# Kernel tuning notes

Hardware: AMD Instinct MI355X
Metric: run time of the kernel (lower is better)

Reference implementation:

```python
import jax, jax.numpy as jnp
import numpy as np

B, C_IN, H, W = 64, 2048, 14, 14
D, FF, G, NC, NH = 768, 2048, 100, 9605, 8
DF = int(NC / G + 0.999)  # 97
HD = D // NH
EPS = 1e-5


def _ln(x, g, b):
    m = jnp.mean(x, axis=-1, keepdims=True)
    v = jnp.mean(jnp.square(x - m), axis=-1, keepdims=True)
    return (x - m) * jax.lax.rsqrt(v + EPS) * g + b


def setup_inputs() -> dict:
    key = jax.random.key(0)
    ks = jax.random.split(key, 16)
    def xav(k, shape):
        fan_in, fan_out = shape[-1], shape[-2] if len(shape) > 1 else shape[-1]
        std = float(np.sqrt(2.0 / (fan_in + fan_out)))
        return jax.random.normal(k, shape, jnp.float32) * std
    return {
        "x": jax.random.normal(ks[0], (B, C_IN, H, W), jnp.float32),
        "w_embed": xav(ks[1], (D, C_IN)), "b_embed": jnp.zeros((D,), jnp.float32),
        "query_embed": jax.random.normal(ks[2], (G, D), jnp.float32),
        "wq": xav(ks[3], (D, D)), "bq": jnp.zeros((D,), jnp.float32),
        "wk": xav(ks[4], (D, D)), "bk": jnp.zeros((D,), jnp.float32),
        "wv": xav(ks[5], (D, D)), "bv": jnp.zeros((D,), jnp.float32),
        "wo": xav(ks[6], (D, D)), "bo": jnp.zeros((D,), jnp.float32),
        "g1": jnp.ones((D,), jnp.float32), "be1": jnp.zeros((D,), jnp.float32),
        "g2": jnp.ones((D,), jnp.float32), "be2": jnp.zeros((D,), jnp.float32),
        "g3": jnp.ones((D,), jnp.float32), "be3": jnp.zeros((D,), jnp.float32),
        "w1": xav(ks[7], (FF, D)), "bl1": jnp.zeros((FF,), jnp.float32),
        "w2": xav(ks[8], (D, FF)), "bl2": jnp.zeros((D,), jnp.float32),
        "dup_pool": xav(ks[9], (G, D, DF)),
        "dup_bias": jnp.zeros((NC,), jnp.float32),
    }


def reference(x, w_embed, b_embed, query_embed, wq, bq, wk, bk, wv, bv, wo, bo,
              g1, be1, g2, be2, g3, be3, w1, bl1, w2, bl2, dup_pool, dup_bias):
    bs = x.shape[0]
    # [B, C, H, W] -> [B, S, C]
    mem = x.reshape(bs, x.shape[1], -1).transpose(0, 2, 1)
    # embed_standart + relu -> [B, S, D]
    mem = jax.nn.relu(jnp.einsum('bsc,dc->bsd', mem, w_embed) + b_embed)
    # tgt = queries broadcast to batch: [B, G, D]
    tgt = jnp.broadcast_to(query_embed[None], (bs, G, D))
    # layer: tgt = norm1(tgt + dropout1(tgt)) = norm1(2*tgt)
    tgt = _ln(tgt + tgt, g1, be1)
    # cross multihead attention (q=tgt, k=v=mem)
    q = (jnp.einsum('bgd,ed->bge', tgt, wq) + bq).reshape(bs, G, NH, HD)
    k = (jnp.einsum('bsd,ed->bse', mem, wk) + bk).reshape(bs, -1, NH, HD)
    v = (jnp.einsum('bsd,ed->bse', mem, wv) + bv).reshape(bs, -1, NH, HD)
    scores = jnp.einsum('bghd,bshd->bhgs', q, k) / jnp.sqrt(jnp.float32(HD))
    attn = jax.nn.softmax(scores, axis=-1)
    ctx = jnp.einsum('bhgs,bshd->bghd', attn, v).reshape(bs, G, D)
    ctx = jnp.einsum('bgd,ed->bge', ctx, wo) + bo
    tgt = _ln(tgt + ctx, g2, be2)
    # FFN
    ff = jax.nn.relu(jnp.einsum('bgd,fd->bgf', tgt, w1) + bl1)
    ff = jnp.einsum('bgf,df->bgd', ff, w2) + bl2
    h = _ln(tgt + ff, g3, be3)  # [B, G, D]
    # grouped FC: per-group matmul fused into one batched einsum
    out_extrap = jnp.einsum('bgd,gdf->bgf', h, dup_pool)  # [B, G, DF]
    logits = out_extrap.reshape(bs, G * DF)[:, :NC] + dup_bias
    return logits
```

## Files before the change

kernel.cpp:

```cpp
#include <hip/hip_runtime.h>
#include <hip/hip_bf16.h>


#define B_    64
#define CIN_  2048
#define S_    196
#define D_    768
#define FF_   2048
#define G_    100
#define NC_   9605
#define NH_   8
#define HD_   96
#define DF_   97
#define FP_   112
#define GP_   112
#define SP_   224
#define BS_   (B_ * S_)
#define BG_   (B_ * G_)

typedef __bf16 bf16x8 __attribute__((ext_vector_type(8)));
typedef float  f32x4  __attribute__((ext_vector_type(4)));
typedef ushort us8    __attribute__((ext_vector_type(8)));

__device__ __forceinline__ float bf2f(ushort u) {
  union { unsigned int i; float f; } v; v.i = ((unsigned int)u) << 16; return v.f;
}
__device__ __forceinline__ ushort f2bf(float f) {
  __hip_bfloat16 h = __float2bfloat16(f);
  return *reinterpret_cast<ushort*>(&h);
}

__device__ __forceinline__ void gl2lds16(const ushort* g, ushort* l) {
  __builtin_amdgcn_global_load_lds((const __attribute__((address_space(1))) unsigned int*)g,
                                   (__attribute__((address_space(3))) unsigned int*)l, 16, 0, 0);
}

#define DT_BLKS 400
#define XP_BLKS 2048
#define CV_BLKS 512
#define TG_BLKS 128

struct PrepArgs {
  const float* x;   ushort* aemb;
  const float* dup; ushort* dupT;
  const float* csrc[7]; ushort* cdst[7]; int cn4[7]; int ctotal;
  const float* qe; const float* g1; const float* be1;
  float* tgt; ushort* tgtB;
};

__global__ __launch_bounds__(256) void k_prep(PrepArgs pa) {
  __shared__ __align__(16) char smem[196 * 72 * 2];
  int jid = blockIdx.x;
  const int t = threadIdx.x;

  if (jid < DT_BLKS) {
    float (*tile)[33] = (float (*)[33])smem;
    const int g = jid >> 2, dchunk = jid & 3;
    const int tx = t & 31, ty = t >> 5;
    for (int di = 0; di < 6; ++di) {
      const int d0 = dchunk * 192 + di * 32;
      for (int f0 = 0; f0 < 128; f0 += 32) {
        #pragma unroll
        for (int r = 0; r < 32; r += 8) {
          int d = d0 + ty + r, f = f0 + tx;
          tile[ty + r][tx] = (f < DF_) ? pa.dup[(size_t)g * D_ * DF_ + (size_t)d * DF_ + f] : 0.f;
        }
        __syncthreads();
        #pragma unroll
        for (int r = 0; r < 32; r += 8) {
          int f = f0 + ty + r, d = d0 + tx;
          if (f < FP_) pa.dupT[((size_t)g * FP_ + f) * D_ + d] = f2bf(tile[tx][ty + r]);
        }
        __syncthreads();
      }
    }
    return;
  }
  jid -= DT_BLKS;

  if (jid < XP_BLKS) {
    ushort* xs = (ushort*)smem;
    const int b = jid >> 5, cbase = (jid & 31) * 64;
    const float* xb = pa.x + ((size_t)b * CIN_ + cbase) * S_;
    #pragma unroll
    for (int it = 0; it < 4; ++it) {
      const int u = it * 256 + t;
      if (u < 784) {
        const int cq = u / 49, j = u - cq * 49;
        const int s = 4 * j;
        float4 a[4];
        #pragma unroll
        for (int r = 0; r < 4; ++r)
          a[r] = *(const float4*)(xb + (size_t)(cq * 4 + r) * S_ + s);
        #pragma unroll
        for (int r = 0; r < 4; ++r) {
          ushort4 o;
          o.x = f2bf(((const float*)&a[0])[r]);
          o.y = f2bf(((const float*)&a[1])[r]);
          o.z = f2bf(((const float*)&a[2])[r]);
          o.w = f2bf(((const float*)&a[3])[r]);
          *(ushort4*)&xs[(s + r) * 72 + cq * 4] = o;
        }
      }
    }
    __syncthreads();
    const int sl = t >> 3, oct = t & 7;
    #pragma unroll
    for (int sr = 0; sr < 7; ++sr) {
      const int s = sr * 32 + sl;
      if (s < S_) {
        us8 v = *(const us8*)&xs[s * 72 + oct * 8];
        *(us8*)&pa.aemb[((size_t)(b * S_ + s)) * CIN_ + cbase + oct * 8] = v;
      }
    }
    return;
  }
  jid -= XP_BLKS;

  if (jid < CV_BLKS) {
    int i = jid * 256 + t;
    const int stride = CV_BLKS * 256;
    for (; i < pa.ctotal; i += stride) {
      int seg = 0, off = i;
      while (off >= pa.cn4[seg]) { off -= pa.cn4[seg]; ++seg; }
      const float4* sp = (const float4*)pa.csrc[seg];
      float4 v0 = sp[2 * off], v1 = sp[2 * off + 1];
      us8 o;
      o[0] = f2bf(v0.x); o[1] = f2bf(v0.y); o[2] = f2bf(v0.z); o[3] = f2bf(v0.w);
      o[4] = f2bf(v1.x); o[5] = f2bf(v1.y); o[6] = f2bf(v1.z); o[7] = f2bf(v1.w);
      ((us8*)pa.cdst[seg])[off] = o;
    }
    return;
  }
  jid -= CV_BLKS;

  float* r1 = (float*)smem;
  float* r2 = r1 + 256;
  const int g = jid;
  if (g >= G_) {
    for (int d = t; d < D_; d += 256) pa.tgtB[(size_t)g * D_ + d] = 0;
    return;
  }
  float y[3]; float s = 0.f, sq = 0.f;
  const float* row = pa.qe + (size_t)g * D_;
  #pragma unroll
  for (int i = 0; i < 3; ++i) { float v = 2.f * row[t + i * 256]; y[i] = v; s += v; sq += v * v; }
  r1[t] = s; r2[t] = sq; __syncthreads();
  for (int o = 128; o > 0; o >>= 1) { if (t < o) { r1[t] += r1[t + o]; r2[t] += r2[t + o]; } __syncthreads(); }
  const float mean = r1[0] * (1.f / D_);
  const float var  = r2[0] * (1.f / D_) - mean * mean;
  const float w = rsqrtf(var + 1e-5f);
  #pragma unroll
  for (int i = 0; i < 3; ++i) {
    int d = t + i * 256;
    float v = (y[i] - mean) * w * pa.g1[d] + pa.be1[d];
    pa.tgt[(size_t)g * D_ + d] = v;
    pa.tgtB[(size_t)g * D_ + d] = f2bf(v);
  }
}

__device__ __forceinline__ void gemm_core(const ushort* __restrict__ A, const ushort* __restrict__ B,
    const float* __restrict__ bias, const float* __restrict__ bias2,
    float* __restrict__ Cf, ushort* __restrict__ Cb, ushort* __restrict__ Vt,
    int N, int K, int m0, int n0, int relu, ushort* As, ushort* Bs) {
  const int t = threadIdx.x;
  const int lane = t & 63, wave = t >> 6;
  const int quad = lane >> 4, lrow = lane & 15;
  const int wr = (wave >> 1) * 64, wc = (wave & 1) * 64;
  const int srow = t >> 2, scol = (t & 3) * 8;
  f32x4 acc[4][4] = {};
  for (int k0 = 0; k0 < K; k0 += 32) {
    const ushort* ag = A + (size_t)(m0 + srow) * K + k0 + scol;
    const ushort* bg = B + (size_t)(n0 + srow) * K + k0 + scol;
    gl2lds16(ag,                    &As[srow * 32 + scol]);
    gl2lds16(ag + (size_t)64 * K,   &As[(srow + 64) * 32 + scol]);
    gl2lds16(bg,                    &Bs[srow * 32 + scol]);
    gl2lds16(bg + (size_t)64 * K,   &Bs[(srow + 64) * 32 + scol]);
    __syncthreads();
    bf16x8 af[4], bfr[4];
    #pragma unroll
    for (int i = 0; i < 4; ++i) af[i] = *(const bf16x8*)&As[(wr + i * 16 + lrow) * 32 + quad * 8];
    #pragma unroll
    for (int j = 0; j < 4; ++j) bfr[j] = *(const bf16x8*)&Bs[(wc + j * 16 + lrow) * 32 + quad * 8];
    #pragma unroll
    for (int i = 0; i < 4; ++i)
      #pragma unroll
      for (int j = 0; j < 4; ++j)
        acc[i][j] = __builtin_amdgcn_mfma_f32_16x16x32_bf16(af[i], bfr[j], acc[i][j], 0, 0, 0);
    __syncthreads();
  }
  #pragma unroll
  for (int i = 0; i < 4; ++i) {
    #pragma unroll
    for (int j = 0; j < 4; ++j) {
      const int gcol = n0 + wc + j * 16 + lrow;
      const float bv = (bias2 && gcol >= D_) ? bias2[gcol - D_] : (bias ? bias[gcol] : 0.f);
      if (Vt && gcol >= D_) {
        const int dv = gcol - D_, hh = dv / HD_, hd = dv % HD_;
        const int row0 = m0 + wr + i * 16 + quad * 4;
        const int bb = row0 / S_, ss = row0 % S_;
        ushort4 o;
        o.x = f2bf(acc[i][j][0] + bv);
        o.y = f2bf(acc[i][j][1] + bv);
        o.z = f2bf(acc[i][j][2] + bv);
        o.w = f2bf(acc[i][j][3] + bv);
        *(ushort4*)&Vt[((size_t)(bb * NH_ + hh) * HD_ + hd) * SP_ + ss] = o;
      } else {
        #pragma unroll
        for (int r = 0; r < 4; ++r) {
          const int grow = m0 + wr + i * 16 + quad * 4 + r;
          float v = acc[i][j][r] + bv;
          if (relu) v = fmaxf(v, 0.f);
          if (Cf) Cf[(size_t)grow * N + gcol] = v;
          else    Cb[(size_t)grow * N + gcol] = f2bf(v);
        }
      }
    }
  }
}

__global__ __launch_bounds__(256) void k_gemm(const ushort* __restrict__ A, const ushort* __restrict__ B,
    const float* __restrict__ bias, const float* __restrict__ bias2,
    float* __restrict__ Cf, ushort* __restrict__ Cb, ushort* __restrict__ Vt,
    int N, int K, int nbx, int nm, int relu,
    const ushort* __restrict__ A2, const ushort* __restrict__ B2,
    const float* __restrict__ bias_2, ushort* __restrict__ Cb2, int N2, int K2) {
  __shared__ ushort As[128 * 32];
  __shared__ ushort Bs[128 * 32];
  const int l = blockIdx.x;
  const int base = ((nm + 7) & ~7) * nbx;
  if (l >= base) {
    gemm_core(A2, B2, bias_2, nullptr, nullptr, Cb2, nullptr, N2, K2, 0, (l - base) * 128, 0, As, Bs);
    return;
  }
  const int mb = (l >> 3) / nbx * 8 + (l & 7);
  const int nb = (l >> 3) % nbx;
  if (mb >= nm) return;
  gemm_core(A, B, bias, bias2, Cf, Cb, Vt, N, K, mb * 128, nb * 128, relu, As, Bs);
}
static inline int swz_grid(int nm, int nbx) { return ((nm + 7) & ~7) * nbx; }

__device__ __forceinline__ void gemm_core64(const ushort* __restrict__ A, const ushort* __restrict__ B,
    const float* __restrict__ bias, ushort* __restrict__ Cb,
    int N, int K, int m0, int n0, int relu, ushort* As, ushort* Bs) {
  const int t = threadIdx.x;
  const int lane = t & 63, wave = t >> 6;
  const int quad = lane >> 4, lrow = lane & 15;
  const int wr = (wave >> 1) * 32, wc = (wave & 1) * 64;
  const int srow = t >> 2, scol = (t & 3) * 8;
  f32x4 acc[2][4] = {};
  for (int k0 = 0; k0 < K; k0 += 32) {
    const ushort* ag = A + (size_t)(m0 + srow) * K + k0 + scol;
    const ushort* bg = B + (size_t)(n0 + srow) * K + k0 + scol;
    gl2lds16(ag,                  &As[srow * 32 + scol]);
    gl2lds16(bg,                  &Bs[srow * 32 + scol]);
    gl2lds16(bg + (size_t)64 * K, &Bs[(srow + 64) * 32 + scol]);
    __syncthreads();
    bf16x8 af[2], bfr[4];
    #pragma unroll
    for (int i = 0; i < 2; ++i) af[i] = *(const bf16x8*)&As[(wr + i * 16 + lrow) * 32 + quad * 8];
    #pragma unroll
    for (int j = 0; j < 4; ++j) bfr[j] = *(const bf16x8*)&Bs[(wc + j * 16 + lrow) * 32 + quad * 8];
    #pragma unroll
    for (int i = 0; i < 2; ++i)
      #pragma unroll
      for (int j = 0; j < 4; ++j)
        acc[i][j] = __builtin_amdgcn_mfma_f32_16x16x32_bf16(af[i], bfr[j], acc[i][j], 0, 0, 0);
    __syncthreads();
  }
  #pragma unroll
  for (int i = 0; i < 2; ++i) {
    #pragma unroll
    for (int j = 0; j < 4; ++j) {
      const int gcol = n0 + wc + j * 16 + lrow;
      const float bv = bias ? bias[gcol] : 0.f;
      #pragma unroll
      for (int r = 0; r < 4; ++r) {
        const int grow = m0 + wr + i * 16 + quad * 4 + r;
        float v = acc[i][j][r] + bv;
        if (relu) v = fmaxf(v, 0.f);
        Cb[(size_t)grow * N + gcol] = f2bf(v);
      }
    }
  }
}

__global__ __launch_bounds__(256) void k_gemm64(const ushort* __restrict__ A, const ushort* __restrict__ B,
    const float* __restrict__ bias, ushort* __restrict__ Cb,
    int N, int K, int nbx, int nm, int relu,
    const ushort* __restrict__ A2, const ushort* __restrict__ B2,
    const float* __restrict__ bias_2, ushort* __restrict__ Cb2, int N2, int K2, int nbx2) {
  __shared__ ushort As[64 * 32];
  __shared__ ushort Bs[128 * 32];
  const int l = blockIdx.x;
  const int base = ((nm + 7) & ~7) * nbx;
  if (l >= base) {
    const int l2 = l - base;
    gemm_core64(A2, B2, bias_2, Cb2, N2, K2, (l2 / nbx2) * 64, (l2 % nbx2) * 128, 0, As, Bs);
    return;
  }
  const int mb = (l >> 3) / nbx * 8 + (l & 7);
  const int nb = (l >> 3) % nbx;
  if (mb >= nm) return;
  gemm_core64(A, B, bias, Cb, N, K, mb * 64, nb * 128, relu, As, Bs);
}

__global__ __launch_bounds__(256) void k_attn(const ushort* __restrict__ qB,
    const ushort* __restrict__ Kb, const ushort* __restrict__ VbT, ushort* __restrict__ ctx) {
  __shared__ ushort lds[GP_ * SP_];
  ushort* Ks = lds;
  ushort* Ps = lds;
  const int h = blockIdx.x, b = blockIdx.y, t = threadIdx.x;
  const int bh = b * NH_ + h;
  const int lane = t & 63, wave = t >> 6;
  const int quad = lane >> 4, c = lane & 15;
  for (int i = t; i < 208 * 12; i += 256) {
    int r = i / 12, col = (i % 12) * 8;
    gl2lds16(Kb + ((size_t)(b * S_ + r)) * D_ + h * HD_ + col, &Ks[i * 8]);
  }
  __syncthreads();
  const float scale = 0.1020620726f;
  f32x4 p[2][13];
  #pragma unroll
  for (int rep = 0; rep < 2; ++rep) {
    const int ii = wave + rep * 4;
    if (ii >= 7) continue;
    bf16x8 af[3];
    #pragma unroll
    for (int ks = 0; ks < 3; ++ks)
      af[ks] = *(const bf16x8*)(qB + ((size_t)(ii * 16 + c)) * D_ + h * HD_ + ks * 32 + quad * 8);
    #pragma unroll
    for (int j = 0; j < 13; ++j) {
      f32x4 a = {};
      #pragma unroll
      for (int ks = 0; ks < 3; ++ks) {
        bf16x8 bf = *(const bf16x8*)&Ks[(j * 16 + c) * HD_ + ks * 32 + quad * 8];
        a = __builtin_amdgcn_mfma_f32_16x16x32_bf16(af[ks], bf, a, 0, 0, 0);
      }
      p[rep][j] = a;
    }
    float m[4] = {-1e30f, -1e30f, -1e30f, -1e30f};
    #pragma unroll
    for (int j = 0; j < 13; ++j)
      #pragma unroll
      for (int r = 0; r < 4; ++r) {
        float v = p[rep][j][r] * scale;
        if (j == 12 && c >= 4) v = -1e30f;
        p[rep][j][r] = v;
        m[r] = fmaxf(m[r], v);
      }
    #pragma unroll
    for (int r = 0; r < 4; ++r) {
      m[r] = fmaxf(m[r], __shfl_xor(m[r], 1));
      m[r] = fmaxf(m[r], __shfl_xor(m[r], 2));
      m[r] = fmaxf(m[r], __shfl_xor(m[r], 4));
      m[r] = fmaxf(m[r], __shfl_xor(m[r], 8));
    }
    float lsum[4] = {0.f, 0.f, 0.f, 0.f};
    #pragma unroll
    for (int j = 0; j < 13; ++j)
      #pragma unroll
      for (int r = 0; r < 4; ++r) {
        float e = __expf(p[rep][j][r] - m[r]);
        p[rep][j][r] = e; lsum[r] += e;
      }
    #pragma unroll
    for (int r = 0; r < 4; ++r) {
      lsum[r] += __shfl_xor(lsum[r], 1);
      lsum[r] += __shfl_xor(lsum[r], 2);
      lsum[r] += __shfl_xor(lsum[r], 4);
      lsum[r] += __shfl_xor(lsum[r], 8);
      lsum[r] = 1.f / lsum[r];
    }
    #pragma unroll
    for (int j = 0; j < 13; ++j)
      #pragma unroll
      for (int r = 0; r < 4; ++r)
        p[rep][j][r] *= lsum[r];
  }
  __syncthreads();
  #pragma unroll
  for (int rep = 0; rep < 2; ++rep) {
    const int ii = wave + rep * 4;
    if (ii >= 7) continue;
    #pragma unroll
    for (int r = 0; r < 4; ++r) {
      const int g = ii * 16 + quad * 4 + r;
      #pragma unroll
      for (int j = 0; j < 13; ++j)
        Ps[g * SP_ + j * 16 + c] = f2bf(p[rep][j][r]);
      Ps[g * SP_ + 208 + c] = 0;
    }
  }
  __syncthreads();
  #pragma unroll
  for (int rep = 0; rep < 2; ++rep) {
    const int ii = wave + rep * 4;
    if (ii >= 7) continue;
    bf16x8 af[7];
    #pragma unroll
    for (int k = 0; k < 7; ++k)
      af[k] = *(const bf16x8*)&Ps[(ii * 16 + c) * SP_ + k * 32 + quad * 8];
    #pragma unroll
    for (int j = 0; j < 6; ++j) {
      f32x4 acc = {};
      #pragma unroll
      for (int k = 0; k < 7; ++k) {
        bf16x8 bf = *(const bf16x8*)(VbT + ((size_t)bh * HD_ + j * 16 + c) * SP_ + k * 32 + quad * 8);
        acc = __builtin_amdgcn_mfma_f32_16x16x32_bf16(af[k], bf, acc, 0, 0, 0);
      }
      #pragma unroll
      for (int r = 0; r < 4; ++r) {
        const int g = ii * 16 + quad * 4 + r;
        if (g < G_)
          ctx[((size_t)(b * G_ + g)) * D_ + h * HD_ + j * 16 + c] = f2bf(acc[r]);
      }
    }
  }
}

__global__ __launch_bounds__(256) void k_lnres(const float* __restrict__ resid, int resid_mod,
    const ushort* __restrict__ addB, const float* __restrict__ gamma, const float* __restrict__ beta,
    float* __restrict__ outf, ushort* __restrict__ outb, int transb) {
  const int row = blockIdx.x, t = threadIdx.x;
  __shared__ float r1[256], r2[256];
  const float* rrow = resid + (size_t)(resid_mod ? (row % G_) : row) * D_;
  const ushort* arow = addB + (size_t)row * D_;
  float y[3]; float s = 0.f, sq = 0.f;
  #pragma unroll
  for (int i = 0; i < 3; ++i) {
    int d = t + i * 256;
    float v = rrow[d] + bf2f(arow[d]);
    y[i] = v; s += v; sq += v * v;
  }
  r1[t] = s; r2[t] = sq; __syncthreads();
  for (int o = 128; o > 0; o >>= 1) { if (t < o) { r1[t] += r1[t + o]; r2[t] += r2[t + o]; } __syncthreads(); }
  const float mean = r1[0] * (1.f / D_);
  const float var  = r2[0] * (1.f / D_) - mean * mean;
  const float w = rsqrtf(var + 1e-5f);
  const size_t orow = transb ? ((size_t)(row % G_) * B_ + row / G_) : (size_t)row;
  #pragma unroll
  for (int i = 0; i < 3; ++i) {
    int d = t + i * 256;
    float v = (y[i] - mean) * w * gamma[d] + beta[d];
    if (outf) outf[(size_t)row * D_ + d] = v;
    if (outb) outb[orow * D_ + d] = f2bf(v);
  }
}

__global__ __launch_bounds__(256) void k_head4(const ushort* __restrict__ hT,
    const ushort* __restrict__ dupT, const float* __restrict__ dup_bias, float* __restrict__ out) {
  const int g = blockIdx.x, j = blockIdx.y, t = threadIdx.x;
  const int lane = t & 63, wave = t >> 6;
  const int quad = lane >> 4, c = lane & 15;
  const ushort* ap = hT + ((size_t)g * B_ + wave * 16 + c) * D_;
  const ushort* bp = dupT + ((size_t)g * FP_ + j * 16 + c) * D_;
  f32x4 acc = {};
  #pragma unroll 8
  for (int k0 = 0; k0 < D_; k0 += 32) {
    bf16x8 af = *(const bf16x8*)(ap + k0 + quad * 8);
    bf16x8 bf = *(const bf16x8*)(bp + k0 + quad * 8);
    acc = __builtin_amdgcn_mfma_f32_16x16x32_bf16(af, bf, acc, 0, 0, 0);
  }
  const int f = j * 16 + c;
  if (f >= DF_) return;
  const int n = g * DF_ + f;
  if (n >= NC_) return;
  const float bv = dup_bias[n];
  #pragma unroll
  for (int r = 0; r < 4; ++r) {
    const int b = wave * 16 + quad * 4 + r;
    out[(size_t)b * NC_ + n] = acc[r] + bv;
  }
}

static constexpr size_t OFF_AEMB  = 0;
static constexpr size_t OFF_VBT   = 0;
static constexpr size_t OFF_FF    = 0;
static constexpr size_t OFF_FFO   = 26214400;
static constexpr size_t OFF_WEMB  = 51380224;
static constexpr size_t OFF_MEM   = 54525952;
static constexpr size_t OFF_WK    = 73793536;
static constexpr size_t OFF_WV    = 74973184;
static constexpr size_t OFF_WO    = 76152832;
static constexpr size_t OFF_W1    = 77332480;
static constexpr size_t OFF_W2    = 80478208;
static constexpr size_t OFF_DUP   = 83623936;
static constexpr size_t OFF_KB    = 100827136;
static constexpr size_t OFF_TGT   = 139362304;
static constexpr size_t OFF_TGTB  = 139669504;
static constexpr size_t OFF_Q     = 139866112;
static constexpr size_t OFF_CTX   = 140068864;
static constexpr size_t OFF_WQ    = OFF_CTX;
static constexpr size_t OFF_CTXO  = 149899264;
static constexpr size_t OFF_TGT2F = 169560064;
static constexpr size_t OFF_TGT2B = 189220864;
static constexpr size_t OFF_HB    = 199051264;

extern "C" void kernel_launch(void* const* d_in, const int* in_sizes, int n_in,
                              void* d_out, int out_size, void* d_ws, size_t ws_size,
                              hipStream_t stream) {
  const float* x           = (const float*)d_in[0];
  const float* w_embed     = (const float*)d_in[1];
  const float* b_embed     = (const float*)d_in[2];
  const float* query_embed = (const float*)d_in[3];
  const float* wq          = (const float*)d_in[4];
  const float* bq          = (const float*)d_in[5];
  const float* wk          = (const float*)d_in[6];
  const float* bk          = (const float*)d_in[7];
  const float* wv          = (const float*)d_in[8];
  const float* bv          = (const float*)d_in[9];
  const float* wo          = (const float*)d_in[10];
  const float* bo          = (const float*)d_in[11];
  const float* g1          = (const float*)d_in[12];
  const float* be1         = (const float*)d_in[13];
  const float* g2          = (const float*)d_in[14];
  const float* be2         = (const float*)d_in[15];
  const float* g3          = (const float*)d_in[16];
  const float* be3         = (const float*)d_in[17];
  const float* w1          = (const float*)d_in[18];
  const float* bl1         = (const float*)d_in[19];
  const float* w2          = (const float*)d_in[20];
  const float* bl2         = (const float*)d_in[21];
  const float* dup_pool    = (const float*)d_in[22];
  const float* dup_bias    = (const float*)d_in[23];
  float* out = (float*)d_out;
  char* ws = (char*)d_ws;

  ushort* aemb  = (ushort*)(ws + OFF_AEMB);
  ushort* wembB = (ushort*)(ws + OFF_WEMB);
  ushort* memB  = (ushort*)(ws + OFF_MEM);
  ushort* wkvB  = (ushort*)(ws + OFF_WK);
  ushort* wkB   = (ushort*)(ws + OFF_WK);
  ushort* wvB   = (ushort*)(ws + OFF_WV);
  ushort* woB   = (ushort*)(ws + OFF_WO);
  ushort* w1B   = (ushort*)(ws + OFF_W1);
  ushort* w2B   = (ushort*)(ws + OFF_W2);
  ushort* wqB   = (ushort*)(ws + OFF_WQ);
  ushort* dupT  = (ushort*)(ws + OFF_DUP);
  ushort* Kb    = (ushort*)(ws + OFF_KB);
  float*  tgtF  = (float*)(ws + OFF_TGT);
  ushort* tgtB  = (ushort*)(ws + OFF_TGTB);
  ushort* qB    = (ushort*)(ws + OFF_Q);
  ushort* VbT   = (ushort*)(ws + OFF_VBT);
  ushort* ctxB  = (ushort*)(ws + OFF_CTX);
  ushort* ctxoB = (ushort*)(ws + OFF_CTXO);
  float*  tgt2F = (float*)(ws + OFF_TGT2F);
  ushort* tgt2B = (ushort*)(ws + OFF_TGT2B);
  ushort* ffB   = (ushort*)(ws + OFF_FF);
  ushort* ffoB  = (ushort*)(ws + OFF_FFO);
  ushort* hT    = (ushort*)(ws + OFF_HB);

  PrepArgs pa;
  pa.x = x; pa.aemb = aemb;
  pa.dup = dup_pool; pa.dupT = dupT;
  pa.csrc[0] = w_embed; pa.cdst[0] = wembB; pa.cn4[0] = D_ * CIN_ / 8;
  pa.csrc[1] = wk;      pa.cdst[1] = wkB;   pa.cn4[1] = D_ * D_ / 8;
  pa.csrc[2] = wv;      pa.cdst[2] = wvB;   pa.cn4[2] = D_ * D_ / 8;
  pa.csrc[3] = wo;      pa.cdst[3] = woB;   pa.cn4[3] = D_ * D_ / 8;
  pa.csrc[4] = w1;      pa.cdst[4] = w1B;   pa.cn4[4] = FF_ * D_ / 8;
  pa.csrc[5] = w2;      pa.cdst[5] = w2B;   pa.cn4[5] = D_ * FF_ / 8;
  pa.csrc[6] = wq;      pa.cdst[6] = wqB;   pa.cn4[6] = D_ * D_ / 8;
  pa.ctotal = pa.cn4[0] + pa.cn4[1] + pa.cn4[2] + pa.cn4[3] + pa.cn4[4] + pa.cn4[5] + pa.cn4[6];
  pa.qe = query_embed; pa.g1 = g1; pa.be1 = be1; pa.tgt = tgtF; pa.tgtB = tgtB;
  k_prep<<<DT_BLKS + XP_BLKS + CV_BLKS + TG_BLKS, 256, 0, stream>>>(pa);

  k_gemm64<<<swz_grid(196, 6) + 12, 256, 0, stream>>>(aemb, wembB, b_embed, memB,
                                                      D_, CIN_, 6, 196, 1,
                                                      tgtB, wqB, bq, qB, D_, D_, 6);

  k_gemm<<<swz_grid(98, 12), 256, 0, stream>>>(memB, wkvB, bk, bv, nullptr, Kb, VbT,
                                               D_, D_, 12, 98, 0,
                                               nullptr, nullptr, nullptr, nullptr, 0, 0);

  k_attn<<<dim3(NH_, B_), 256, 0, stream>>>(qB, Kb, VbT, ctxB);

  k_gemm64<<<swz_grid(100, 6), 256, 0, stream>>>(ctxB, woB, bo, ctxoB,
                                                 D_, D_, 6, 100, 0,
                                                 nullptr, nullptr, nullptr, nullptr, 0, 0, 1);

  k_lnres<<<BG_, 256, 0, stream>>>(tgtF, 1, ctxoB, g2, be2, tgt2F, tgt2B, 0);

  k_gemm<<<swz_grid(50, 16), 256, 0, stream>>>(tgt2B, w1B, bl1, nullptr, nullptr, ffB, nullptr,
                                               FF_, D_, 16, 50, 1,
                                               nullptr, nullptr, nullptr, nullptr, 0, 0);
  k_gemm64<<<swz_grid(100, 6), 256, 0, stream>>>(ffB, w2B, bl2, ffoB,
                                                 D_, FF_, 6, 100, 0,
                                                 nullptr, nullptr, nullptr, nullptr, 0, 0, 1);

  k_lnres<<<BG_, 256, 0, stream>>>(tgt2F, 0, ffoB, g3, be3, nullptr, hT, 1);

  k_head4<<<dim3(G_, 7), 256, 0, stream>>>(hT, dupT, dup_bias, out);
}
```

Baseline: 568.6 us.

## Double-buffer LDS tiles in GEMM cores and reorder x-transpose indexing

Both GEMM cores now keep two LDS buffers per operand. The next K-tile's global-to-LDS load is issued before the MFMA work on the current tile, leaving one barrier per iteration instead of two, so load latency overlaps compute. LDS use per block doubles, which may lower occupancy. The input transpose block also swaps its work-index decomposition so consecutive threads vary the channel quad instead of the spatial index, changing its global access pattern.

```diff
diff --git a/kernel.cpp b/kernel.cpp
--- a/kernel.cpp
+++ b/kernel.cpp
@@ -86,7 +86,7 @@
     for (int it = 0; it < 4; ++it) {
       const int u = it * 256 + t;
       if (u < 784) {
-        const int cq = u / 49, j = u - cq * 49;
+        const int j = u >> 4, cq = u & 15;
         const int s = 4 * j;
         float4 a[4];
         #pragma unroll
@@ -168,26 +168,39 @@
   const int quad = lane >> 4, lrow = lane & 15;
   const int wr = (wave >> 1) * 64, wc = (wave & 1) * 64;
   const int srow = t >> 2, scol = (t & 3) * 8;
+  const ushort* ag = A + (size_t)(m0 + srow) * K + scol;
+  const ushort* bg = B + (size_t)(n0 + srow) * K + scol;
+  ushort* asw = As + t * 8;
+  ushort* bsw = Bs + t * 8;
   f32x4 acc[4][4] = {};
+  gl2lds16(ag,                  asw);
+  gl2lds16(ag + (size_t)64 * K, asw + 64 * 32);
+  gl2lds16(bg,                  bsw);
+  gl2lds16(bg + (size_t)64 * K, bsw + 64 * 32);
+  __syncthreads();
+  int cur = 0;
   for (int k0 = 0; k0 < K; k0 += 32) {
-    const ushort* ag = A + (size_t)(m0 + srow) * K + k0 + scol;
-    const ushort* bg = B + (size_t)(n0 + srow) * K + k0 + scol;
-    gl2lds16(ag,                    &As[srow * 32 + scol]);
-    gl2lds16(ag + (size_t)64 * K,   &As[(srow + 64) * 32 + scol]);
-    gl2lds16(bg,                    &Bs[srow * 32 + scol]);
-    gl2lds16(bg + (size_t)64 * K,   &Bs[(srow + 64) * 32 + scol]);
-    __syncthreads();
+    if (k0 + 32 < K) {
+      const int nb = (cur ^ 1) * (128 * 32);
+      gl2lds16(ag + k0 + 32,                  asw + nb);
+      gl2lds16(ag + k0 + 32 + (size_t)64 * K, asw + nb + 64 * 32);
+      gl2lds16(bg + k0 + 32,                  bsw + nb);
+      gl2lds16(bg + k0 + 32 + (size_t)64 * K, bsw + nb + 64 * 32);
+    }
+    const ushort* as = As + cur * (128 * 32);
+    const ushort* bs = Bs + cur * (128 * 32);
     bf16x8 af[4], bfr[4];
     #pragma unroll
-    for (int i = 0; i < 4; ++i) af[i] = *(const bf16x8*)&As[(wr + i * 16 + lrow) * 32 + quad * 8];
-    #pragma unroll
-    for (int j = 0; j < 4; ++j) bfr[j] = *(const bf16x8*)&Bs[(wc + j * 16 + lrow) * 32 + quad * 8];
+    for (int i = 0; i < 4; ++i) af[i] = *(const bf16x8*)&as[(wr + i * 16 + lrow) * 32 + quad * 8];
+    #pragma unroll
+    for (int j = 0; j < 4; ++j) bfr[j] = *(const bf16x8*)&bs[(wc + j * 16 + lrow) * 32 + quad * 8];
     #pragma unroll
     for (int i = 0; i < 4; ++i)
       #pragma unroll
       for (int j = 0; j < 4; ++j)
         acc[i][j] = __builtin_amdgcn_mfma_f32_16x16x32_bf16(af[i], bfr[j], acc[i][j], 0, 0, 0);
     __syncthreads();
+    cur ^= 1;
   }
   #pragma unroll
   for (int i = 0; i < 4; ++i) {
@@ -225,8 +238,8 @@
     int N, int K, int nbx, int nm, int relu,
     const ushort* __restrict__ A2, const ushort* __restrict__ B2,
     const float* __restrict__ bias_2, ushort* __restrict__ Cb2, int N2, int K2) {
-  __shared__ ushort As[128 * 32];
-  __shared__ ushort Bs[128 * 32];
+  __shared__ ushort As[2 * 128 * 32];
+  __shared__ ushort Bs[2 * 128 * 32];
   const int l = blockIdx.x;
   const int base = ((nm + 7) & ~7) * nbx;
   if (l >= base) {
@@ -248,25 +261,36 @@
   const int quad = lane >> 4, lrow = lane & 15;
   const int wr = (wave >> 1) * 32, wc = (wave & 1) * 64;
   const int srow = t >> 2, scol = (t & 3) * 8;
+  const ushort* ag = A + (size_t)(m0 + srow) * K + scol;
+  const ushort* bg = B + (size_t)(n0 + srow) * K + scol;
+  ushort* asw = As + t * 8;
+  ushort* bsw = Bs + t * 8;
   f32x4 acc[2][4] = {};
+  gl2lds16(ag,                  asw);
+  gl2lds16(bg,                  bsw);
+  gl2lds16(bg + (size_t)64 * K, bsw + 64 * 32);
+  __syncthreads();
+  int cur = 0;
   for (int k0 = 0; k0 < K; k0 += 32) {
-    const ushort* ag = A + (size_t)(m0 + srow) * K + k0 + scol;
-    const ushort* bg = B + (size_t)(n0 + srow) * K + k0 + scol;
-    gl2lds16(ag,                  &As[srow * 32 + scol]);
-    gl2lds16(bg,                  &Bs[srow * 32 + scol]);
-    gl2lds16(bg + (size_t)64 * K, &Bs[(srow + 64) * 32 + scol]);
-    __syncthreads();
+    if (k0 + 32 < K) {
+      gl2lds16(ag + k0 + 32,                  asw + (cur ^ 1) * (64 * 32));
+      gl2lds16(bg + k0 + 32,                  bsw + (cur ^ 1) * (128 * 32));
+      gl2lds16(bg + k0 + 32 + (size_t)64 * K, bsw + (cur ^ 1) * (128 * 32) + 64 * 32);
+    }
+    const ushort* as = As + cur * (64 * 32);
+    const ushort* bs = Bs + cur * (128 * 32);
     bf16x8 af[2], bfr[4];
     #pragma unroll
-    for (int i = 0; i < 2; ++i) af[i] = *(const bf16x8*)&As[(wr + i * 16 + lrow) * 32 + quad * 8];
-    #pragma unroll
-    for (int j = 0; j < 4; ++j) bfr[j] = *(const bf16x8*)&Bs[(wc + j * 16 + lrow) * 32 + quad * 8];
+    for (int i = 0; i < 2; ++i) af[i] = *(const bf16x8*)&as[(wr + i * 16 + lrow) * 32 + quad * 8];
+    #pragma unroll
+    for (int j = 0; j < 4; ++j) bfr[j] = *(const bf16x8*)&bs[(wc + j * 16 + lrow) * 32 + quad * 8];
     #pragma unroll
     for (int i = 0; i < 2; ++i)
       #pragma unroll
       for (int j = 0; j < 4; ++j)
         acc[i][j] = __builtin_amdgcn_mfma_f32_16x16x32_bf16(af[i], bfr[j], acc[i][j], 0, 0, 0);
     __syncthreads();
+    cur ^= 1;
   }
   #pragma unroll
   for (int i = 0; i < 2; ++i) {
@@ -290,8 +314,8 @@
     int N, int K, int nbx, int nm, int relu,
     const ushort* __restrict__ A2, const ushort* __restrict__ B2,
     const float* __restrict__ bias_2, ushort* __restrict__ Cb2, int N2, int K2, int nbx2) {
-  __shared__ ushort As[64 * 32];
-  __shared__ ushort Bs[128 * 32];
+  __shared__ ushort As[2 * 64 * 32];
+  __shared__ ushort Bs[2 * 128 * 32];
   const int l = blockIdx.x;
   const int base = ((nm + 7) & ~7) * nbx;
   if (l >= base) {
```

New measurement: 558.8 us. No clear change (-1.7%).
